# Optimization experiments

Measured on AMD Instinct MI355X. Metric: run time of the kernel, lower is better.

The kernel has to match this reference:

```python
import jax, jax.numpy as jnp
import numpy as np
import math

D = 128  # hidden_dim
N_USERS = 10000
N_ITEMS = 12000
NEG_INF = -9e15


def setup_inputs() -> dict:
    key = jax.random.key(0)
    k1, k2, k3, k4, k5 = jax.random.split(key, 5)
    ufea = jax.random.normal(k1, (N_USERS, D), dtype=jnp.float32)
    inter = jax.random.normal(k2, (N_ITEMS, D), dtype=jnp.float32)
    adj = jax.random.randint(k3, (N_USERS, N_ITEMS), 0, 2, dtype=jnp.int32)
    # linear layer params (torch default init approximated with scaled normals)
    W = jax.random.normal(k4, (D, D), dtype=jnp.float32) / jnp.sqrt(jnp.float32(D))
    b = jax.random.normal(k5, (D,), dtype=jnp.float32) * 0.01
    return {"ufea": ufea, "inter": inter, "adj": adj, "W": W, "b": b}


def _leaky_relu2(x):
    # nn.LeakyReLU(2): negative_slope = 2
    return jnp.where(x > 0, x, 2.0 * x)


def reference(ufea, inter, adj, W, b):
    # GAT.forward_user with dropout in eval mode (identity).
    # Attention.forward(a=ufea, b=inter, adj)
    query = ufea @ W.T + b                      # [N, D]  nn.Linear
    scale = 1.0 / math.sqrt(D)
    scores = _leaky_relu2((query @ inter.T) * scale)   # [N, M]
    scores = jnp.where(adj > 0, scores, NEG_INF)        # mask non-edges
    attn = jax.nn.softmax(scores, axis=1)               # row softmax
    result = attn @ inter                                # [N, D]
    return result
```

## Files before the change

kernel.cpp:

```cpp
#include <hip/hip_runtime.h>
#include <cstdint>
#include <cstddef>


#define N_USERS 10000
#define N_ITEMS 12000
#define HD      128
#define QROWS   10048
#define NCHUNK  8
#define NTILES  188
#define UBLOCKS 157
#define KT_PITCH 12032

typedef __bf16 bf16x8 __attribute__((ext_vector_type(8)));
typedef __bf16 bf16x4 __attribute__((ext_vector_type(4)));
typedef float  f32x4  __attribute__((ext_vector_type(4)));
typedef int    i32x4  __attribute__((ext_vector_type(4)));

typedef const __attribute__((address_space(1))) unsigned int g_u32;
typedef __attribute__((address_space(3))) unsigned int l_u32;

__global__ __launch_bounds__(256) void cast_inter_kernel(const float* __restrict__ inter,
                                                         __bf16* __restrict__ kg,
                                                         __bf16* __restrict__ ktg) {
    __shared__ __bf16 Tl[128 * 72];
    const int t  = threadIdx.x;
    const int i0 = blockIdx.x * 64;
    for (int it = 0; it < 8; ++it) {
        int g   = it * 256 + t;
        int row = g >> 5;
        int d   = (g & 31) * 4;
        int item = i0 + row;
        if (item < N_ITEMS) {
            f32x4 v = *(const f32x4*)(inter + (size_t)item * HD + d);
            __bf16 b0 = (__bf16)v.x, b1 = (__bf16)v.y, b2 = (__bf16)v.z, b3 = (__bf16)v.w;
            bf16x4 pk = {b0, b1, b2, b3};
            *(bf16x4*)(kg + (size_t)item * HD + d) = pk;
            Tl[(d + 0) * 72 + row] = b0;
            Tl[(d + 1) * 72 + row] = b1;
            Tl[(d + 2) * 72 + row] = b2;
            Tl[(d + 3) * 72 + row] = b3;
        } else {
            Tl[(d + 0) * 72 + row] = (__bf16)0.f;
            Tl[(d + 1) * 72 + row] = (__bf16)0.f;
            Tl[(d + 2) * 72 + row] = (__bf16)0.f;
            Tl[(d + 3) * 72 + row] = (__bf16)0.f;
        }
    }
    __syncthreads();
    const int d  = t >> 1;
    const int jb = (t & 1) * 32;
    if (i0 + jb < N_ITEMS) {
        #pragma unroll
        for (int k = 0; k < 4; ++k) {
            bf16x8 v = *(const bf16x8*)&Tl[d * 72 + jb + k * 8];
            *(bf16x8*)(ktg + (size_t)d * KT_PITCH + i0 + jb + k * 8) = v;
        }
    }
}

__global__ __launch_bounds__(256) void query_kernel(const float* __restrict__ ufea,
                                                    const float* __restrict__ W,
                                                    const float* __restrict__ bias,
                                                    __bf16* __restrict__ qg) {
    const int lane = threadIdx.x & 63, wave = threadIdx.x >> 6;
    const int n = lane & 15, qd = lane >> 4;
    const int user0 = blockIdx.x * 64 + wave * 16;
    int arow = user0 + n; if (arow > N_USERS - 1) arow = N_USERS - 1;

    bf16x8 af[4];
    #pragma unroll
    for (int kk = 0; kk < 4; ++kk) {
        const float* p = ufea + (size_t)arow * HD + kk * 32 + qd * 8;
        f32x4 lo = *(const f32x4*)p, hi = *(const f32x4*)(p + 4);
        bf16x8 a;
        a[0]=(__bf16)lo.x; a[1]=(__bf16)lo.y; a[2]=(__bf16)lo.z; a[3]=(__bf16)lo.w;
        a[4]=(__bf16)hi.x; a[5]=(__bf16)hi.y; a[6]=(__bf16)hi.z; a[7]=(__bf16)hi.w;
        af[kk] = a;
    }
    #pragma unroll
    for (int nt = 0; nt < 8; ++nt) {
        f32x4 acc = {0.f, 0.f, 0.f, 0.f};
        #pragma unroll
        for (int kk = 0; kk < 4; ++kk) {
            const float* p = W + (size_t)(nt * 16 + n) * HD + kk * 32 + qd * 8;
            f32x4 lo = *(const f32x4*)p, hi = *(const f32x4*)(p + 4);
            bf16x8 b;
            b[0]=(__bf16)lo.x; b[1]=(__bf16)lo.y; b[2]=(__bf16)lo.z; b[3]=(__bf16)lo.w;
            b[4]=(__bf16)hi.x; b[5]=(__bf16)hi.y; b[6]=(__bf16)hi.z; b[7]=(__bf16)hi.w;
            acc = __builtin_amdgcn_mfma_f32_16x16x32_bf16(af[kk], b, acc, 0, 0, 0);
        }
        const float bv = bias[nt * 16 + n];
        #pragma unroll
        for (int r = 0; r < 4; ++r) {
            int row = user0 + qd * 4 + r;
            qg[(size_t)row * HD + nt * 16 + n] = (__bf16)(acc[r] + bv);
        }
    }
}

__global__ __launch_bounds__(256) void fused_kernel(const __bf16* __restrict__ qg,
                                                    const __bf16* __restrict__ kg,
                                                    const __bf16* __restrict__ ktg,
                                                    const int* __restrict__ adj,
                                                    float* __restrict__ Opart,
                                                    float* __restrict__ lpart) {
    __shared__ __bf16 Kbuf[16 * 512];
    __shared__ __bf16 Vbuf[16 * 512];
    __shared__ __bf16 Pl[4][16 * 72];
    __shared__ unsigned int Al[4][272];
    const int lane = threadIdx.x & 63, wave = threadIdx.x >> 6;
    const int n = lane & 15, qd = lane >> 4;
    const int user0 = blockIdx.x * 64 + wave * 16;
    const int chunk = blockIdx.y;
    const int t0 = (chunk * NTILES) / NCHUNK;
    const int t1 = ((chunk + 1) * NTILES) / NCHUNK;
    const float SC = (float)(1.4426950408889634 * 0.08838834764831845);

    bf16x8 qf[4];
    #pragma unroll
    for (int kk = 0; kk < 4; ++kk)
        qf[kk] = *(const bf16x8*)(qg + (size_t)(user0 + n) * HD + kk * 32 + qd * 8);

    f32x4 Oacc[8];
    #pragma unroll
    for (int dt = 0; dt < 8; ++dt) Oacc[dt] = (f32x4){0.f, 0.f, 0.f, 0.f};
    float lacc[4] = {0.f, 0.f, 0.f, 0.f};

    size_t adjOff[4];
    #pragma unroll
    for (int r = 0; r < 4; ++r) {
        int u = user0 + qd * 4 + r;
        if (u > N_USERS - 1) u = N_USERS - 1;
        adjOff[r] = (size_t)u * N_ITEMS;
    }
    __bf16* pw = &Pl[wave][0];
    unsigned int* aw = &Al[wave][0];

    i32x4 av[4];
    {
        int c = t0 * 64 + n * 4; if (c > N_ITEMS - 4) c = N_ITEMS - 4;
        #pragma unroll
        for (int r = 0; r < 4; ++r)
            av[r] = __builtin_nontemporal_load((const i32x4*)(adj + adjOff[r] + c));
    }

    for (int t = t0; t < t1; ++t) {
        const int j0 = t * 64;
        __syncthreads();

        #pragma unroll
        for (int j = 0; j < 4; ++j) {
            const int c  = wave * 4 + j;
            const int nt = c >> 2, kk = c & 3;
            int item = j0 + nt * 16 + n; if (item > N_ITEMS - 1) item = N_ITEMS - 1;
            const __bf16* src = kg + (size_t)item * HD + kk * 32 + qd * 8;
            __builtin_amdgcn_global_load_lds((g_u32*)src, (l_u32*)(Kbuf + c * 512), 16, 0, 0);
        }
        #pragma unroll
        for (int j = 0; j < 4; ++j) {
            const int c  = wave * 4 + j;
            const int dt = c >> 1, kc = c & 1;
            const __bf16* src = ktg + (size_t)(dt * 16 + n) * KT_PITCH + j0 + kc * 32 + qd * 8;
            __builtin_amdgcn_global_load_lds((g_u32*)src, (l_u32*)(Vbuf + c * 512), 16, 0, 0);
        }

        #pragma unroll
        for (int cc = 0; cc < 4; ++cc) {
            unsigned int packed = (unsigned int)av[0][cc] | ((unsigned int)av[1][cc] << 8)
                                | ((unsigned int)av[2][cc] << 16) | ((unsigned int)av[3][cc] << 24);
            aw[qd * 68 + n * 4 + cc] = packed;
        }
        if (t + 1 < t1) {
            int c = (t + 1) * 64 + n * 4; if (c > N_ITEMS - 4) c = N_ITEMS - 4;
            #pragma unroll
            for (int r = 0; r < 4; ++r)
                av[r] = __builtin_nontemporal_load((const i32x4*)(adj + adjOff[r] + c));
        }

        __syncthreads();

        f32x4 S[4];
        #pragma unroll
        for (int nt = 0; nt < 4; ++nt) S[nt] = (f32x4){0.f, 0.f, 0.f, 0.f};
        #pragma unroll
        for (int nt = 0; nt < 4; ++nt) {
            #pragma unroll
            for (int kk = 0; kk < 4; ++kk) {
                bf16x8 b = *(const bf16x8*)(Kbuf + (nt * 4 + kk) * 512 + (qd * 16 + n) * 8);
                S[nt] = __builtin_amdgcn_mfma_f32_16x16x32_bf16(qf[kk], b, S[nt], 0, 0, 0);
            }
        }
        #pragma unroll
        for (int nt = 0; nt < 4; ++nt) {
            const int col = j0 + nt * 16 + n;
            const bool cv = col < N_ITEMS;
            const unsigned int m = aw[qd * 68 + nt * 16 + n];
            #pragma unroll
            for (int r = 0; r < 4; ++r) {
                float s = S[nt][r] * SC;
                s = fminf(s, s + s);
                const bool on = cv && ((m >> (8 * r)) & 1u);
                float p = on ? __builtin_amdgcn_exp2f(s) : 0.f;
                lacc[r] += p;
                pw[(qd * 4 + r) * 72 + nt * 16 + n] = (__bf16)p;
            }
        }
        #pragma unroll
        for (int kc = 0; kc < 2; ++kc) {
            bf16x8 af = *(const bf16x8*)(pw + n * 72 + kc * 32 + qd * 8);
            #pragma unroll
            for (int dt = 0; dt < 8; ++dt) {
                bf16x8 b = *(const bf16x8*)(Vbuf + (dt * 2 + kc) * 512 + (qd * 16 + n) * 8);
                Oacc[dt] = __builtin_amdgcn_mfma_f32_16x16x32_bf16(af, b, Oacc[dt], 0, 0, 0);
            }
        }
    }

    #pragma unroll
    for (int r = 0; r < 4; ++r) {
        float v = lacc[r];
        v += __shfl_xor(v, 1);
        v += __shfl_xor(v, 2);
        v += __shfl_xor(v, 4);
        v += __shfl_xor(v, 8);
        lacc[r] = v;
    }
    const size_t cb = (size_t)chunk * QROWS;
    #pragma unroll
    for (int r = 0; r < 4; ++r) {
        const int user = user0 + qd * 4 + r;
        if (user < N_USERS) {
            #pragma unroll
            for (int dt = 0; dt < 8; ++dt)
                Opart[(cb + user) * HD + dt * 16 + n] = Oacc[dt][r];
            if (n == 0) lpart[cb + user] = lacc[r];
        }
    }
}

__global__ __launch_bounds__(256) void combine_kernel(const float* __restrict__ Opart,
                                                      const float* __restrict__ lpart,
                                                      float* __restrict__ out) {
    const int g = blockIdx.x * 256 + threadIdx.x;
    const int base = g * 4;
    const int user = base >> 7;
    const int d = base & 127;
    f32x4 acc = {0.f, 0.f, 0.f, 0.f};
    float l = 0.f;
    #pragma unroll
    for (int c = 0; c < NCHUNK; ++c) {
        acc += *(const f32x4*)(Opart + ((size_t)c * QROWS + user) * HD + d);
        l += lpart[(size_t)c * QROWS + user];
    }
    f32x4 res = acc / l;
    *(f32x4*)(out + (size_t)user * HD + d) = res;
}

extern "C" void kernel_launch(void* const* d_in, const int* in_sizes, int n_in,
                              void* d_out, int out_size, void* d_ws, size_t ws_size,
                              hipStream_t stream) {
    const float* ufea = (const float*)d_in[0];
    const float* inter = (const float*)d_in[1];
    const int*   adj  = (const int*)d_in[2];
    const float* W    = (const float*)d_in[3];
    const float* bias = (const float*)d_in[4];
    float* out = (float*)d_out;

    char* ws = (char*)d_ws;
    __bf16* qg   = (__bf16*)(ws);
    __bf16* kg   = (__bf16*)(ws + 2572288);
    __bf16* ktg  = (__bf16*)(ws + 2572288 + 3072000);
    float*  Opart = (float*)(ws + 2572288 + 3072000 + 3080192);
    float*  lpart = (float*)(ws + 2572288 + 3072000 + 3080192 + 41156608);

    cast_inter_kernel<<<dim3(188), dim3(256), 0, stream>>>(inter, kg, ktg);
    query_kernel<<<dim3(UBLOCKS), dim3(256), 0, stream>>>(ufea, W, bias, qg);
    fused_kernel<<<dim3(UBLOCKS, NCHUNK), dim3(256), 0, stream>>>(qg, kg, ktg, adj, Opart, lpart);
    combine_kernel<<<dim3(1250), dim3(256), 0, stream>>>(Opart, lpart, out);
}
```

Baseline: 725.1 us.

## Double-buffer K/V tiles, read adjacency directly in registers, split items into more chunks

The K and V tile loads into LDS become double-buffered, so the next tile's global-to-LDS copy is issued before computing on the current one, and one barrier per iteration is removed. The adjacency mask is now loaded as int2 pairs matching a permuted K row order, so masks are used directly from registers instead of being packed through a shared-memory staging array. The item dimension is split into 16 chunks instead of 8, with chunk as the fast grid axis, which raises parallelism but doubles the partial-output traffic for the combine step. The LDS footprint doubles and the partial-buffer workspace offsets grow to match.

```diff
diff --git a/kernel.cpp b/kernel.cpp
--- a/kernel.cpp
+++ b/kernel.cpp
@@ -7,15 +7,17 @@
 #define N_ITEMS 12000
 #define HD      128
 #define QROWS   10048
-#define NCHUNK  8
+#define NCHUNK  16
+#define TILE    64
 #define NTILES  188
 #define UBLOCKS 157
 #define KT_PITCH 12032
 
 typedef __bf16 bf16x8 __attribute__((ext_vector_type(8)));
 typedef __bf16 bf16x4 __attribute__((ext_vector_type(4)));
+typedef __bf16 bf16x2 __attribute__((ext_vector_type(2)));
 typedef float  f32x4  __attribute__((ext_vector_type(4)));
-typedef int    i32x4  __attribute__((ext_vector_type(4)));
+typedef int    i32x2  __attribute__((ext_vector_type(2)));
 
 typedef const __attribute__((address_space(1))) unsigned int g_u32;
 typedef __attribute__((address_space(3))) unsigned int l_u32;
@@ -99,20 +101,19 @@
     }
 }
 
-__global__ __launch_bounds__(256) void fused_kernel(const __bf16* __restrict__ qg,
-                                                    const __bf16* __restrict__ kg,
-                                                    const __bf16* __restrict__ ktg,
-                                                    const int* __restrict__ adj,
-                                                    float* __restrict__ Opart,
-                                                    float* __restrict__ lpart) {
-    __shared__ __bf16 Kbuf[16 * 512];
-    __shared__ __bf16 Vbuf[16 * 512];
+__global__ __launch_bounds__(256, 2) void fused_kernel(const __bf16* __restrict__ qg,
+                                                       const __bf16* __restrict__ kg,
+                                                       const __bf16* __restrict__ ktg,
+                                                       const int* __restrict__ adj,
+                                                       float* __restrict__ Opart,
+                                                       float* __restrict__ lpart) {
+    __shared__ __bf16 Kbuf[2][16 * 512];
+    __shared__ __bf16 Vbuf[2][16 * 512];
     __shared__ __bf16 Pl[4][16 * 72];
-    __shared__ unsigned int Al[4][272];
     const int lane = threadIdx.x & 63, wave = threadIdx.x >> 6;
     const int n = lane & 15, qd = lane >> 4;
-    const int user0 = blockIdx.x * 64 + wave * 16;
-    const int chunk = blockIdx.y;
+    const int user0 = blockIdx.y * 64 + wave * 16;
+    const int chunk = blockIdx.x;
     const int t0 = (chunk * NTILES) / NCHUNK;
     const int t1 = ((chunk + 1) * NTILES) / NCHUNK;
     const float SC = (float)(1.4426950408889634 * 0.08838834764831845);
@@ -135,50 +136,50 @@
         adjOff[r] = (size_t)u * N_ITEMS;
     }
     __bf16* pw = &Pl[wave][0];
-    unsigned int* aw = &Al[wave][0];
-
-    i32x4 av[4];
-    {
-        int c = t0 * 64 + n * 4; if (c > N_ITEMS - 4) c = N_ITEMS - 4;
-        #pragma unroll
-        for (int r = 0; r < 4; ++r)
-            av[r] = __builtin_nontemporal_load((const i32x4*)(adj + adjOff[r] + c));
-    }
+
+    auto stage = [&](int t, int b) {
+        const int j0s = t * TILE;
+        #pragma unroll
+        for (int j = 0; j < 4; ++j) {
+            const int c = wave * 4 + j;
+            int row = j0s + (wave >> 1) * 32 + 2 * n + (wave & 1);
+            if (row > N_ITEMS - 1) row = N_ITEMS - 1;
+            const __bf16* src = kg + (size_t)row * HD + j * 32 + qd * 8;
+            __builtin_amdgcn_global_load_lds((g_u32*)src, (l_u32*)(&Kbuf[b][c * 512]), 16, 0, 0);
+        }
+        #pragma unroll
+        for (int j = 0; j < 4; ++j) {
+            const int c = wave * 4 + j;
+            const int dt = c >> 1, kc = c & 1;
+            const __bf16* src = ktg + (size_t)(dt * 16 + n) * KT_PITCH + j0s + kc * 32 + qd * 8;
+            __builtin_amdgcn_global_load_lds((g_u32*)src, (l_u32*)(&Vbuf[b][c * 512]), 16, 0, 0);
+        }
+    };
+    auto load_adj = [&](int t, i32x2 av[2][4]) {
+        #pragma unroll
+        for (int h = 0; h < 2; ++h) {
+            int col2 = t * TILE + h * 32 + 2 * n;
+            if (col2 > N_ITEMS - 2) col2 = N_ITEMS - 2;
+            #pragma unroll
+            for (int r = 0; r < 4; ++r)
+                av[h][r] = __builtin_nontemporal_load((const i32x2*)(adj + adjOff[r] + col2));
+        }
+    };
+
+    stage(t0, 0);
+    i32x2 av[2][4];
+    load_adj(t0, av);
 
     for (int t = t0; t < t1; ++t) {
-        const int j0 = t * 64;
+        const int cur = (t - t0) & 1;
+        const int j0 = t * TILE;
         __syncthreads();
 
-        #pragma unroll
-        for (int j = 0; j < 4; ++j) {
-            const int c  = wave * 4 + j;
-            const int nt = c >> 2, kk = c & 3;
-            int item = j0 + nt * 16 + n; if (item > N_ITEMS - 1) item = N_ITEMS - 1;
-            const __bf16* src = kg + (size_t)item * HD + kk * 32 + qd * 8;
-            __builtin_amdgcn_global_load_lds((g_u32*)src, (l_u32*)(Kbuf + c * 512), 16, 0, 0);
-        }
-        #pragma unroll
-        for (int j = 0; j < 4; ++j) {
-            const int c  = wave * 4 + j;
-            const int dt = c >> 1, kc = c & 1;
-            const __bf16* src = ktg + (size_t)(dt * 16 + n) * KT_PITCH + j0 + kc * 32 + qd * 8;
-            __builtin_amdgcn_global_load_lds((g_u32*)src, (l_u32*)(Vbuf + c * 512), 16, 0, 0);
-        }
-
-        #pragma unroll
-        for (int cc = 0; cc < 4; ++cc) {
-            unsigned int packed = (unsigned int)av[0][cc] | ((unsigned int)av[1][cc] << 8)
-                                | ((unsigned int)av[2][cc] << 16) | ((unsigned int)av[3][cc] << 24);
-            aw[qd * 68 + n * 4 + cc] = packed;
-        }
+        i32x2 avn[2][4];
         if (t + 1 < t1) {
-            int c = (t + 1) * 64 + n * 4; if (c > N_ITEMS - 4) c = N_ITEMS - 4;
-            #pragma unroll
-            for (int r = 0; r < 4; ++r)
-                av[r] = __builtin_nontemporal_load((const i32x4*)(adj + adjOff[r] + c));
-        }
-
-        __syncthreads();
+            load_adj(t + 1, avn);
+            stage(t + 1, cur ^ 1);
+        }
 
         f32x4 S[4];
         #pragma unroll
@@ -187,23 +188,28 @@
         for (int nt = 0; nt < 4; ++nt) {
             #pragma unroll
             for (int kk = 0; kk < 4; ++kk) {
-                bf16x8 b = *(const bf16x8*)(Kbuf + (nt * 4 + kk) * 512 + (qd * 16 + n) * 8);
+                bf16x8 b = *(const bf16x8*)(&Kbuf[cur][(nt * 4 + kk) * 512 + lane * 8]);
                 S[nt] = __builtin_amdgcn_mfma_f32_16x16x32_bf16(qf[kk], b, S[nt], 0, 0, 0);
             }
         }
         #pragma unroll
-        for (int nt = 0; nt < 4; ++nt) {
-            const int col = j0 + nt * 16 + n;
-            const bool cv = col < N_ITEMS;
-            const unsigned int m = aw[qd * 68 + nt * 16 + n];
-            #pragma unroll
-            for (int r = 0; r < 4; ++r) {
-                float s = S[nt][r] * SC;
-                s = fminf(s, s + s);
-                const bool on = cv && ((m >> (8 * r)) & 1u);
-                float p = on ? __builtin_amdgcn_exp2f(s) : 0.f;
-                lacc[r] += p;
-                pw[(qd * 4 + r) * 72 + nt * 16 + n] = (__bf16)p;
+        for (int r = 0; r < 4; ++r) {
+            #pragma unroll
+            for (int h = 0; h < 2; ++h) {
+                const int colb = j0 + h * 32 + 2 * n;
+                float p01[2];
+                #pragma unroll
+                for (int par = 0; par < 2; ++par) {
+                    const int nt = h * 2 + par;
+                    float s = S[nt][r] * SC;
+                    s = fminf(s, s + s);
+                    const bool on = (colb + par < N_ITEMS) && (av[h][r][par] > 0);
+                    float p = on ? __builtin_amdgcn_exp2f(s) : 0.f;
+                    lacc[r] += p;
+                    p01[par] = p;
+                }
+                bf16x2 pk = {(__bf16)p01[0], (__bf16)p01[1]};
+                *(bf16x2*)(pw + (qd * 4 + r) * 72 + h * 32 + 2 * n) = pk;
             }
         }
         #pragma unroll
@@ -211,10 +217,15 @@
             bf16x8 af = *(const bf16x8*)(pw + n * 72 + kc * 32 + qd * 8);
             #pragma unroll
             for (int dt = 0; dt < 8; ++dt) {
-                bf16x8 b = *(const bf16x8*)(Vbuf + (dt * 2 + kc) * 512 + (qd * 16 + n) * 8);
+                bf16x8 b = *(const bf16x8*)(&Vbuf[cur][(dt * 2 + kc) * 512 + lane * 8]);
                 Oacc[dt] = __builtin_amdgcn_mfma_f32_16x16x32_bf16(af, b, Oacc[dt], 0, 0, 0);
             }
         }
+        #pragma unroll
+        for (int h = 0; h < 2; ++h)
+            #pragma unroll
+            for (int r = 0; r < 4; ++r)
+                av[h][r] = avn[h][r];
     }
 
     #pragma unroll
@@ -270,12 +281,12 @@
     char* ws = (char*)d_ws;
     __bf16* qg   = (__bf16*)(ws);
     __bf16* kg   = (__bf16*)(ws + 2572288);
-    __bf16* ktg  = (__bf16*)(ws + 2572288 + 3072000);
-    float*  Opart = (float*)(ws + 2572288 + 3072000 + 3080192);
-    float*  lpart = (float*)(ws + 2572288 + 3072000 + 3080192 + 41156608);
+    __bf16* ktg  = (__bf16*)(ws + 5644288);
+    float*  Opart = (float*)(ws + 8724480);
+    float*  lpart = (float*)(ws + 91037696);
 
     cast_inter_kernel<<<dim3(188), dim3(256), 0, stream>>>(inter, kg, ktg);
     query_kernel<<<dim3(UBLOCKS), dim3(256), 0, stream>>>(ufea, W, bias, qg);
-    fused_kernel<<<dim3(UBLOCKS, NCHUNK), dim3(256), 0, stream>>>(qg, kg, ktg, adj, Opart, lpart);
+    fused_kernel<<<dim3(NCHUNK, UBLOCKS), dim3(256), 0, stream>>>(qg, kg, ktg, adj, Opart, lpart);
     combine_kernel<<<dim3(1250), dim3(256), 0, stream>>>(Opart, lpart, out);
 }
```

Result: no change. 733.5 us (+1.2%).
